# Performance work log

Hardware: AMD Instinct MI355X
Metric: run time of the kernel (lower is better)

## Reference

```python
import jax, jax.numpy as jnp
import numpy as np

N0, N1, N2 = 20000, 15000, 15000
N = N0 + N1 + N2            # total nodes
E = 800000                  # edges (avg degree 16)
H, C = 128, 64


def setup_inputs() -> dict:
    key = jax.random.key(0)
    ks = jax.random.split(key, 16)
    s = 0.05  # weight scale
    return {
        "feat0": jax.random.normal(ks[0], (N0, 512), jnp.float32),
        "feat1": jax.random.normal(ks[1], (N1, 256), jnp.float32),
        "feat2": jax.random.normal(ks[2], (N2, 128), jnp.float32),
        "W0": jax.random.normal(ks[3], (512, H), jnp.float32) * s,
        "b0": jnp.zeros((H,), jnp.float32),
        "W1": jax.random.normal(ks[4], (256, H), jnp.float32) * s,
        "b1": jnp.zeros((H,), jnp.float32),
        "W2": jax.random.normal(ks[5], (128, H), jnp.float32) * s,
        "b2": jnp.zeros((H,), jnp.float32),
        "bias_l0": jnp.zeros((H,), jnp.float32),
        "W_l1": jax.random.normal(ks[6], (H, H), jnp.float32) * s,
        "b_l1": jnp.zeros((H,), jnp.float32),
        "W_l2": jax.random.normal(ks[7], (H, C), jnp.float32) * s,
        "b_l2": jnp.zeros((C,), jnp.float32),
        "src": jax.random.randint(ks[8], (E,), 0, N, jnp.int32),
        "dst": jax.random.randint(ks[9], (E,), 0, N, jnp.int32),
    }


def _norms(src, dst):
    # DGL GraphConv norm='both': src side uses out-degree, dst side in-degree
    ones = jnp.ones((E,), jnp.float32)
    deg_out = jax.ops.segment_sum(ones, src, num_segments=N)
    deg_in = jax.ops.segment_sum(ones, dst, num_segments=N)
    return jnp.maximum(deg_out, 1.0) ** -0.5, jnp.maximum(deg_in, 1.0) ** -0.5


def _agg(h, src, dst, norm_src, norm_dst):
    # normalized sparse aggregation: D_in^{-1/2} A D_out^{-1/2} h
    m = (h * norm_src[:, None])[src]                     # [E, d] gather
    a = jax.ops.segment_sum(m, dst, num_segments=N)      # [N, d] scatter-add
    return a * norm_dst[:, None]


def reference(feat0, feat1, feat2, W0, b0, W1, b1, W2, b2,
              bias_l0, W_l1, b_l1, W_l2, b_l2, src, dst):
    # per-node-type linear projections, concatenated along node axis
    h = jnp.concatenate([feat0 @ W0 + b0,
                         feat1 @ W1 + b1,
                         feat2 @ W2 + b2], axis=0)       # [N, H]
    ns, nd = _norms(src, dst)
    # layer 0: GraphConv(weight=False) -> agg + bias + relu (dropout = eval identity)
    h = jax.nn.relu(_agg(h, src, dst, ns, nd) + bias_l0)
    # layer 1: agg + linear + relu
    h = jax.nn.relu(_agg(h, src, dst, ns, nd) @ W_l1 + b_l1)
    # layer 2: agg + linear (no activation)
    h = _agg(h, src, dst, ns, nd) @ W_l2 + b_l2          # [N, C]
    return h
```

## Files before the change

kernel.cpp:

```cpp
#include <hip/hip_runtime.h>
#include <hip/hip_fp16.h>

#define N_NODES 50000
#define N0_ 20000
#define N1_ 15000
#define N2_ 15000
#define E_EDGES 800000
#define H_ 128
#define C_ 64

#define PB0 ((N0_ + 63) / 64)
#define PB1 ((N1_ + 63) / 64)
#define PB2 ((N2_ + 63) / 64)
#define PB_TOTAL (PB0 + PB1 + PB2)
#define EB ((E_EDGES + 255) / 256)
#define SB ((N_NODES + 255) / 256)


template <int TN, bool BIAS, bool RELU, bool SCALE, typename OT>
__device__ __forceinline__ void gemm_block(
    const float* __restrict__ A, const float* __restrict__ W,
    const float* __restrict__ bias, const float* __restrict__ rowscale,
    OT* __restrict__ out, int M, int K, int m0, float* As, float* Bs) {
    constexpr int NJ = TN / 32;
    constexpr int TN4 = TN / 4;
    int tid = threadIdx.x;
    int tx = tid & 31;
    int ty = tid >> 5;

    float acc[8][NJ];
#pragma unroll
    for (int i = 0; i < 8; i++)
#pragma unroll
        for (int j = 0; j < NJ; j++) acc[i][j] = 0.f;

    for (int k0 = 0; k0 < K; k0 += 32) {
#pragma unroll
        for (int t0 = 0; t0 < 2; t0++) {
            int t = tid + t0 * 256;
            int row = t >> 3;
            int c = t & 7;
            float4 v = make_float4(0.f, 0.f, 0.f, 0.f);
            if (m0 + row < M) v = *reinterpret_cast<const float4*>(&A[(size_t)(m0 + row) * K + k0 + c * 4]);
            As[(c * 4 + 0) * 68 + row] = v.x;
            As[(c * 4 + 1) * 68 + row] = v.y;
            As[(c * 4 + 2) * 68 + row] = v.z;
            As[(c * 4 + 3) * 68 + row] = v.w;
        }
#pragma unroll
        for (int t0 = 0; t0 < 32 * TN4 / 256; t0++) {
            int t = tid + t0 * 256;
            int r = t / TN4;
            int c4 = t % TN4;
            *reinterpret_cast<float4*>(&Bs[r * TN + c4 * 4]) =
                *reinterpret_cast<const float4*>(&W[(size_t)(k0 + r) * TN + c4 * 4]);
        }
        __syncthreads();
#pragma unroll 8
        for (int k = 0; k < 32; k++) {
            float4 a0 = *reinterpret_cast<float4*>(&As[k * 68 + ty * 8]);
            float4 a1 = *reinterpret_cast<float4*>(&As[k * 68 + ty * 8 + 4]);
            float ar[8] = {a0.x, a0.y, a0.z, a0.w, a1.x, a1.y, a1.z, a1.w};
            float br[NJ];
#pragma unroll
            for (int j = 0; j < NJ; j++) br[j] = Bs[k * TN + tx + 32 * j];
#pragma unroll
            for (int i = 0; i < 8; i++)
#pragma unroll
                for (int j = 0; j < NJ; j++) acc[i][j] = fmaf(ar[i], br[j], acc[i][j]);
        }
        __syncthreads();
    }
#pragma unroll
    for (int i = 0; i < 8; i++) {
        int row = m0 + ty * 8 + i;
        if (row < M) {
            float sc = SCALE ? rowscale[row] : 1.f;
#pragma unroll
            for (int j = 0; j < NJ; j++) {
                float v = acc[i][j] + (BIAS ? bias[tx + 32 * j] : 0.f);
                if (RELU) v = fmaxf(v, 0.f);
                v *= sc;
                out[(size_t)row * TN + tx + 32 * j] = (OT)v;
            }
        }
    }
}


__global__ __launch_bounds__(256) void k1_proj_rank(
    const float* __restrict__ feat0, const float* __restrict__ feat1, const float* __restrict__ feat2,
    const float* __restrict__ W0, const float* __restrict__ b0,
    const float* __restrict__ W1, const float* __restrict__ b1,
    const float* __restrict__ W2, const float* __restrict__ b2,
    __half* __restrict__ h0h,
    const int* __restrict__ src, const int* __restrict__ dst,
    int* __restrict__ cnt, int* __restrict__ degO, int* __restrict__ rank) {
    __shared__ float As[32 * 68];
    __shared__ float Bs[32 * 128];
    int bid = blockIdx.x;
    if (bid < PB_TOTAL) {
        const float* A; const float* Wp; const float* bp; __half* op; int M, K, m0;
        if (bid < PB0) {
            A = feat0; Wp = W0; bp = b0; op = h0h; M = N0_; K = 512; m0 = bid * 64;
        } else if (bid < PB0 + PB1) {
            A = feat1; Wp = W1; bp = b1; op = h0h + (size_t)N0_ * H_; M = N1_; K = 256;
            m0 = (bid - PB0) * 64;
        } else {
            A = feat2; Wp = W2; bp = b2; op = h0h + (size_t)(N0_ + N1_) * H_; M = N2_; K = 128;
            m0 = (bid - PB0 - PB1) * 64;
        }
        gemm_block<128, true, false, false, __half>(A, Wp, bp, nullptr, op, M, K, m0, As, Bs);
    } else {
        int e = (bid - PB_TOTAL) * 256 + threadIdx.x;
        if (e < E_EDGES) {
            rank[e] = atomicAdd(&cnt[dst[e]], 1);
            atomicAdd(&degO[src[e]], 1);
        }
    }
}


__global__ __launch_bounds__(256) void scan1_kernel(
    const int* __restrict__ cnt, int* __restrict__ pre, int* __restrict__ blocksum) {
    __shared__ int buf[256];
    int t = threadIdx.x;
    int i = blockIdx.x * 256 + t;
    int tot = (i < N_NODES) ? cnt[i] : 0;
    buf[t] = tot;
    __syncthreads();
#pragma unroll
    for (int off = 1; off < 256; off <<= 1) {
        int v = (t >= off) ? buf[t - off] : 0;
        __syncthreads();
        buf[t] += v;
        __syncthreads();
    }
    if (i < N_NODES) pre[i] = buf[t] - tot;
    if (t == 255) blocksum[blockIdx.x] = buf[255];
}

__global__ __launch_bounds__(256) void scan2_kernel(
    const int* __restrict__ blocksum, int* __restrict__ blockoff, int* __restrict__ rowptr) {
    __shared__ int buf[256];
    int t = threadIdx.x;
    int v = (t < SB) ? blocksum[t] : 0;
    buf[t] = v;
    __syncthreads();
#pragma unroll
    for (int off = 1; off < 256; off <<= 1) {
        int u = (t >= off) ? buf[t - off] : 0;
        __syncthreads();
        buf[t] += u;
        __syncthreads();
    }
    if (t < SB) blockoff[t] = buf[t] - v;
    if (t == 255) rowptr[N_NODES] = buf[255];
}

__global__ __launch_bounds__(256) void scan3_kernel(
    const int* __restrict__ cnt, const int* __restrict__ degO, const int* __restrict__ pre,
    const int* __restrict__ blockoff, int* __restrict__ rowptr,
    float* __restrict__ ns, float* __restrict__ nd) {
    int i = blockIdx.x * 256 + threadIdx.x;
    if (i < N_NODES) {
        rowptr[i] = blockoff[blockIdx.x] + pre[i];
        ns[i] = rsqrtf(fmaxf((float)degO[i], 1.0f));
        nd[i] = rsqrtf(fmaxf((float)cnt[i], 1.0f));
    }
}


__global__ __launch_bounds__(256) void k2_fill(
    const int* __restrict__ src, const int* __restrict__ dst,
    const int* __restrict__ rowptr, const int* __restrict__ rank,
    int* __restrict__ col) {
    int e = blockIdx.x * 256 + threadIdx.x;
    if (e < E_EDGES) col[rowptr[dst[e]] + rank[e]] = src[e];
}


template <int NSLOAD, int EPI, int OUTH>
__global__ __launch_bounds__(256) void agg_h_kernel(
    const __half* __restrict__ h, const int* __restrict__ rowptr,
    const int* __restrict__ col, const float* __restrict__ ns,
    const float* __restrict__ nd, const float* __restrict__ bias,
    void* __restrict__ out) {
    int node = blockIdx.x * 4 + (threadIdx.x >> 6);
    if (node >= N_NODES) return;
    int lane = threadIdx.x & 63;
    int li = lane & 15;
    int g = lane >> 4;
    const uint4* __restrict__ h8 = (const uint4*)h;
    int beg = rowptr[node], end = rowptr[node + 1];
    float a0[8] = {0.f, 0.f, 0.f, 0.f, 0.f, 0.f, 0.f, 0.f};
    float a1[8] = {0.f, 0.f, 0.f, 0.f, 0.f, 0.f, 0.f, 0.f};
    union U8 { uint4 u; __half2 h2[4]; };
    int e = beg + g;
    for (; e + 4 < end; e += 8) {
        int s0 = col[e], s1 = col[e + 4];
        U8 u0, u1;
        u0.u = h8[(size_t)s0 * 16 + li];
        u1.u = h8[(size_t)s1 * 16 + li];
        float w0 = NSLOAD ? ns[s0] : 1.f;
        float w1 = NSLOAD ? ns[s1] : 1.f;
#pragma unroll
        for (int p = 0; p < 4; p++) {
            float2 f0 = __half22float2(u0.h2[p]);
            float2 f1 = __half22float2(u1.h2[p]);
            if (NSLOAD) {
                a0[2 * p] = fmaf(w0, f0.x, a0[2 * p]);
                a0[2 * p + 1] = fmaf(w0, f0.y, a0[2 * p + 1]);
                a1[2 * p] = fmaf(w1, f1.x, a1[2 * p]);
                a1[2 * p + 1] = fmaf(w1, f1.y, a1[2 * p + 1]);
            } else {
                a0[2 * p] += f0.x;
                a0[2 * p + 1] += f0.y;
                a1[2 * p] += f1.x;
                a1[2 * p + 1] += f1.y;
            }
        }
    }
    if (e < end) {
        int s = col[e];
        U8 u0;
        u0.u = h8[(size_t)s * 16 + li];
        float w0 = NSLOAD ? ns[s] : 1.f;
#pragma unroll
        for (int p = 0; p < 4; p++) {
            float2 f0 = __half22float2(u0.h2[p]);
            if (NSLOAD) {
                a0[2 * p] = fmaf(w0, f0.x, a0[2 * p]);
                a0[2 * p + 1] = fmaf(w0, f0.y, a0[2 * p + 1]);
            } else {
                a0[2 * p] += f0.x;
                a0[2 * p + 1] += f0.y;
            }
        }
    }
#pragma unroll
    for (int j = 0; j < 8; j++) {
        float v = a0[j] + a1[j];
        v += __shfl_xor(v, 32);
        v += __shfl_xor(v, 16);
        a0[j] = v;
    }
    if (lane < 16) {
        float w = nd[node];
#pragma unroll
        for (int j = 0; j < 8; j++) a0[j] *= w;
        if (EPI == 1) {
            float sc = ns[node];
#pragma unroll
            for (int j = 0; j < 8; j++)
                a0[j] = fmaxf(a0[j] + bias[li * 8 + j], 0.f) * sc;
        }
        if (OUTH) {
            union { uint4 u; __half hh[8]; } cv;
#pragma unroll
            for (int j = 0; j < 8; j++) cv.hh[j] = __float2half(a0[j]);
            ((uint4*)out)[(size_t)node * 16 + li] = cv.u;
        } else {
            float4* o4 = (float4*)out;
            o4[(size_t)node * 32 + li * 2] = make_float4(a0[0], a0[1], a0[2], a0[3]);
            o4[(size_t)node * 32 + li * 2 + 1] = make_float4(a0[4], a0[5], a0[6], a0[7]);
        }
    }
}


template <int CH, int NSLOAD, int EPI>
__global__ __launch_bounds__(256) void agg_kernel(
    const float* __restrict__ h, const int* __restrict__ rowptr,
    const int* __restrict__ col, const float* __restrict__ ns,
    const float* __restrict__ nd, const float* __restrict__ bias,
    float* __restrict__ out) {
    constexpr int L = CH / 4;
    constexpr int EPW = 64 / L;
    int node = blockIdx.x * 4 + (threadIdx.x >> 6);
    if (node >= N_NODES) return;
    int lane = threadIdx.x & 63;
    int li = lane & (L - 1);
    int g = lane / L;
    const float4* __restrict__ h4 = (const float4*)h;
    int beg = rowptr[node], end = rowptr[node + 1];
    float4 a0 = make_float4(0.f, 0.f, 0.f, 0.f);
    float4 a1 = a0;
    int e = beg + g;
    for (; e + EPW < end; e += 2 * EPW) {
        int s0 = col[e], s1 = col[e + EPW];
        float4 v0 = h4[(size_t)s0 * L + li];
        float4 v1 = h4[(size_t)s1 * L + li];
        if (NSLOAD) {
            float w0 = ns[s0], w1 = ns[s1];
            a0.x = fmaf(w0, v0.x, a0.x); a0.y = fmaf(w0, v0.y, a0.y);
            a0.z = fmaf(w0, v0.z, a0.z); a0.w = fmaf(w0, v0.w, a0.w);
            a1.x = fmaf(w1, v1.x, a1.x); a1.y = fmaf(w1, v1.y, a1.y);
            a1.z = fmaf(w1, v1.z, a1.z); a1.w = fmaf(w1, v1.w, a1.w);
        } else {
            a0.x += v0.x; a0.y += v0.y; a0.z += v0.z; a0.w += v0.w;
            a1.x += v1.x; a1.y += v1.y; a1.z += v1.z; a1.w += v1.w;
        }
    }
    if (e < end) {
        int s = col[e];
        float4 v = h4[(size_t)s * L + li];
        if (NSLOAD) {
            float w = ns[s];
            a0.x = fmaf(w, v.x, a0.x); a0.y = fmaf(w, v.y, a0.y);
            a0.z = fmaf(w, v.z, a0.z); a0.w = fmaf(w, v.w, a0.w);
        } else {
            a0.x += v.x; a0.y += v.y; a0.z += v.z; a0.w += v.w;
        }
    }
    float4 acc = make_float4(a0.x + a1.x, a0.y + a1.y, a0.z + a1.z, a0.w + a1.w);
#pragma unroll
    for (int off = 32; off >= L; off >>= 1) {
        acc.x += __shfl_xor(acc.x, off);
        acc.y += __shfl_xor(acc.y, off);
        acc.z += __shfl_xor(acc.z, off);
        acc.w += __shfl_xor(acc.w, off);
    }
    if (lane < L) {
        float w = nd[node];
        acc.x *= w; acc.y *= w; acc.z *= w; acc.w *= w;
        if (EPI == 2) {
            float4 b = ((const float4*)bias)[lane];
            acc.x += b.x; acc.y += b.y; acc.z += b.z; acc.w += b.w;
        }
        ((float4*)out)[(size_t)node * L + lane] = acc;
    }
}


template <int TN, bool BIAS, bool RELU, bool SCALE>
__global__ __launch_bounds__(256) void gemm_kernel(
    const float* __restrict__ A, const float* __restrict__ W,
    const float* __restrict__ bias, const float* __restrict__ rowscale,
    float* __restrict__ out, int M, int K) {
    __shared__ float As[32 * 68];
    __shared__ float Bs[32 * TN];
    gemm_block<TN, BIAS, RELU, SCALE, float>(A, W, bias, rowscale, out, M, K, blockIdx.x * 64, As, Bs);
}


extern "C" void kernel_launch(void* const* d_in, const int* in_sizes, int n_in,
                              void* d_out, int out_size, void* d_ws, size_t ws_size,
                              hipStream_t stream) {
    const float* feat0 = (const float*)d_in[0];
    const float* feat1 = (const float*)d_in[1];
    const float* feat2 = (const float*)d_in[2];
    const float* W0 = (const float*)d_in[3];
    const float* b0 = (const float*)d_in[4];
    const float* W1 = (const float*)d_in[5];
    const float* b1 = (const float*)d_in[6];
    const float* W2 = (const float*)d_in[7];
    const float* b2 = (const float*)d_in[8];
    const float* bias_l0 = (const float*)d_in[9];
    const float* W_l1 = (const float*)d_in[10];
    const float* b_l1 = (const float*)d_in[11];
    const float* W_l2 = (const float*)d_in[12];
    const float* b_l2 = (const float*)d_in[13];
    const int* src = (const int*)d_in[14];
    const int* dst = (const int*)d_in[15];
    float* out = (float*)d_out;

    char* ws = (char*)d_ws;
    size_t off = 0;
    auto alloc = [&](size_t bytes) {
        size_t cur = off;
        off += (bytes + 255) & ~(size_t)255;
        return cur;
    };
    size_t hA_off = alloc((size_t)N_NODES * H_ * 4);
    size_t hB_off = alloc((size_t)N_NODES * H_ * 4);
    size_t h0h_off = alloc((size_t)N_NODES * H_ * 2);
    size_t h1h_off = alloc((size_t)N_NODES * H_ * 2);
    size_t cnt_off = alloc((size_t)N_NODES * 4);
    size_t degO_off = alloc((size_t)N_NODES * 4);
    size_t ns_off = alloc((size_t)N_NODES * 4);
    size_t nd_off = alloc((size_t)N_NODES * 4);
    size_t rowptr_off = alloc((size_t)(N_NODES + 1) * 4);
    size_t rank_off = alloc((size_t)E_EDGES * 4);
    size_t col_off = alloc((size_t)E_EDGES * 4);
    size_t pre_off = alloc((size_t)N_NODES * 4);
    size_t bsum_off = alloc((size_t)SB * 4);
    size_t boff_off = alloc((size_t)SB * 4);

    float* hA = (float*)(ws + hA_off);
    float* hB = (float*)(ws + hB_off);
    __half* h0h = (__half*)(ws + h0h_off);
    __half* h1h = (__half*)(ws + h1h_off);
    int* cnt = (int*)(ws + cnt_off);
    int* degO = (int*)(ws + degO_off);
    float* ns = (float*)(ws + ns_off);
    float* nd = (float*)(ws + nd_off);
    int* rowptr = (int*)(ws + rowptr_off);
    int* rank = (int*)(ws + rank_off);
    int* col = (int*)(ws + col_off);
    int* pre = (int*)(ws + pre_off);
    int* bsum = (int*)(ws + bsum_off);
    int* boff = (int*)(ws + boff_off);

    hipMemsetAsync(ws + cnt_off, 0, ns_off - cnt_off, stream);

    k1_proj_rank<<<PB_TOTAL + EB, 256, 0, stream>>>(
        feat0, feat1, feat2, W0, b0, W1, b1, W2, b2, h0h, src, dst, cnt, degO, rank);
    scan1_kernel<<<SB, 256, 0, stream>>>(cnt, pre, bsum);
    scan2_kernel<<<1, 256, 0, stream>>>(bsum, boff, rowptr);
    scan3_kernel<<<SB, 256, 0, stream>>>(cnt, degO, pre, boff, rowptr, ns, nd);
    k2_fill<<<EB, 256, 0, stream>>>(src, dst, rowptr, rank, col);

    const int AGB = (N_NODES + 3) / 4;
    agg_h_kernel<1, 1, 1><<<AGB, 256, 0, stream>>>(h0h, rowptr, col, ns, nd, bias_l0, h1h);
    agg_h_kernel<0, 0, 0><<<AGB, 256, 0, stream>>>(h1h, rowptr, col, ns, nd, nullptr, hA);
    gemm_kernel<128, true, true, true><<<(N_NODES + 63) / 64, 256, 0, stream>>>(
        hA, W_l1, b_l1, ns, hB, N_NODES, 128);
    gemm_kernel<64, false, false, false><<<(N_NODES + 63) / 64, 256, 0, stream>>>(
        hB, W_l2, nullptr, nullptr, hA, N_NODES, 128);
    agg_kernel<64, 0, 2><<<AGB, 256, 0, stream>>>(hA, rowptr, col, ns, nd, b_l2, out);
}
```

Measured before the change: 269.3 us.

## Enlarge GEMM row tiles to 128 and store layer-2 features in half precision

```diff
diff --git a/kernel.cpp b/kernel.cpp
--- a/kernel.cpp
+++ b/kernel.cpp
@@ -9,9 +9,9 @@
 #define H_ 128
 #define C_ 64
 
-#define PB0 ((N0_ + 63) / 64)
-#define PB1 ((N1_ + 63) / 64)
-#define PB2 ((N2_ + 63) / 64)
+#define PB0 ((N0_ + 127) / 128)
+#define PB1 ((N1_ + 127) / 128)
+#define PB2 ((N2_ + 127) / 128)
 #define PB_TOTAL (PB0 + PB1 + PB2)
 #define EB ((E_EDGES + 255) / 256)
 #define SB ((N_NODES + 255) / 256)
@@ -22,11 +22,11 @@
     const float* __restrict__ A, const float* __restrict__ W,
     const float* __restrict__ bias, const float* __restrict__ rowscale,
     OT* __restrict__ out, int M, int K, int m0, float* As, float* Bs) {
-    constexpr int NJ = TN / 32;
+    constexpr int NJ = TN / 16;
     constexpr int TN4 = TN / 4;
     int tid = threadIdx.x;
-    int tx = tid & 31;
-    int ty = tid >> 5;
+    int tx = tid & 15;
+    int ty = tid >> 4;
 
     float acc[8][NJ];
 #pragma unroll
@@ -36,16 +36,16 @@
 
     for (int k0 = 0; k0 < K; k0 += 32) {
 #pragma unroll
-        for (int t0 = 0; t0 < 2; t0++) {
+        for (int t0 = 0; t0 < 4; t0++) {
             int t = tid + t0 * 256;
             int row = t >> 3;
             int c = t & 7;
             float4 v = make_float4(0.f, 0.f, 0.f, 0.f);
             if (m0 + row < M) v = *reinterpret_cast<const float4*>(&A[(size_t)(m0 + row) * K + k0 + c * 4]);
-            As[(c * 4 + 0) * 68 + row] = v.x;
-            As[(c * 4 + 1) * 68 + row] = v.y;
-            As[(c * 4 + 2) * 68 + row] = v.z;
-            As[(c * 4 + 3) * 68 + row] = v.w;
+            As[(c * 4 + 0) * 132 + row] = v.x;
+            As[(c * 4 + 1) * 132 + row] = v.y;
+            As[(c * 4 + 2) * 132 + row] = v.z;
+            As[(c * 4 + 3) * 132 + row] = v.w;
         }
 #pragma unroll
         for (int t0 = 0; t0 < 32 * TN4 / 256; t0++) {
@@ -58,12 +58,12 @@
         __syncthreads();
 #pragma unroll 8
         for (int k = 0; k < 32; k++) {
-            float4 a0 = *reinterpret_cast<float4*>(&As[k * 68 + ty * 8]);
-            float4 a1 = *reinterpret_cast<float4*>(&As[k * 68 + ty * 8 + 4]);
+            float4 a0 = *reinterpret_cast<float4*>(&As[k * 132 + ty * 8]);
+            float4 a1 = *reinterpret_cast<float4*>(&As[k * 132 + ty * 8 + 4]);
             float ar[8] = {a0.x, a0.y, a0.z, a0.w, a1.x, a1.y, a1.z, a1.w};
             float br[NJ];
 #pragma unroll
-            for (int j = 0; j < NJ; j++) br[j] = Bs[k * TN + tx + 32 * j];
+            for (int j = 0; j < NJ; j++) br[j] = Bs[k * TN + tx + 16 * j];
 #pragma unroll
             for (int i = 0; i < 8; i++)
 #pragma unroll
@@ -78,10 +78,10 @@
             float sc = SCALE ? rowscale[row] : 1.f;
 #pragma unroll
             for (int j = 0; j < NJ; j++) {
-                float v = acc[i][j] + (BIAS ? bias[tx + 32 * j] : 0.f);
+                float v = acc[i][j] + (BIAS ? bias[tx + 16 * j] : 0.f);
                 if (RELU) v = fmaxf(v, 0.f);
                 v *= sc;
-                out[(size_t)row * TN + tx + 32 * j] = (OT)v;
+                out[(size_t)row * TN + tx + 16 * j] = (OT)v;
             }
         }
     }
@@ -96,19 +96,19 @@
     __half* __restrict__ h0h,
     const int* __restrict__ src, const int* __restrict__ dst,
     int* __restrict__ cnt, int* __restrict__ degO, int* __restrict__ rank) {
-    __shared__ float As[32 * 68];
+    __shared__ float As[32 * 132];
     __shared__ float Bs[32 * 128];
     int bid = blockIdx.x;
     if (bid < PB_TOTAL) {
         const float* A; const float* Wp; const float* bp; __half* op; int M, K, m0;
         if (bid < PB0) {
-            A = feat0; Wp = W0; bp = b0; op = h0h; M = N0_; K = 512; m0 = bid * 64;
+            A = feat0; Wp = W0; bp = b0; op = h0h; M = N0_; K = 512; m0 = bid * 128;
         } else if (bid < PB0 + PB1) {
             A = feat1; Wp = W1; bp = b1; op = h0h + (size_t)N0_ * H_; M = N1_; K = 256;
-            m0 = (bid - PB0) * 64;
+            m0 = (bid - PB0) * 128;
         } else {
             A = feat2; Wp = W2; bp = b2; op = h0h + (size_t)(N0_ + N1_) * H_; M = N2_; K = 128;
-            m0 = (bid - PB0 - PB1) * 64;
+            m0 = (bid - PB0 - PB1) * 128;
         }
         gemm_block<128, true, false, false, __half>(A, Wp, bp, nullptr, op, M, K, m0, As, Bs);
     } else {
@@ -180,28 +180,30 @@
 }
 
 
-template <int NSLOAD, int EPI, int OUTH>
+template <int CH, int NSLOAD, int EPI, int OUTH>
 __global__ __launch_bounds__(256) void agg_h_kernel(
     const __half* __restrict__ h, const int* __restrict__ rowptr,
     const int* __restrict__ col, const float* __restrict__ ns,
     const float* __restrict__ nd, const float* __restrict__ bias,
     void* __restrict__ out) {
+    constexpr int L = CH / 8;
+    constexpr int EPW = 64 / L;
     int node = blockIdx.x * 4 + (threadIdx.x >> 6);
     if (node >= N_NODES) return;
     int lane = threadIdx.x & 63;
-    int li = lane & 15;
-    int g = lane >> 4;
+    int li = lane & (L - 1);
+    int g = lane / L;
     const uint4* __restrict__ h8 = (const uint4*)h;
     int beg = rowptr[node], end = rowptr[node + 1];
     float a0[8] = {0.f, 0.f, 0.f, 0.f, 0.f, 0.f, 0.f, 0.f};
     float a1[8] = {0.f, 0.f, 0.f, 0.f, 0.f, 0.f, 0.f, 0.f};
     union U8 { uint4 u; __half2 h2[4]; };
     int e = beg + g;
-    for (; e + 4 < end; e += 8) {
-        int s0 = col[e], s1 = col[e + 4];
+    for (; e + EPW < end; e += 2 * EPW) {
+        int s0 = col[e], s1 = col[e + EPW];
         U8 u0, u1;
-        u0.u = h8[(size_t)s0 * 16 + li];
-        u1.u = h8[(size_t)s1 * 16 + li];
+        u0.u = h8[(size_t)s0 * L + li];
+        u1.u = h8[(size_t)s1 * L + li];
         float w0 = NSLOAD ? ns[s0] : 1.f;
         float w1 = NSLOAD ? ns[s1] : 1.f;
 #pragma unroll
@@ -224,7 +226,7 @@
     if (e < end) {
         int s = col[e];
         U8 u0;
-        u0.u = h8[(size_t)s * 16 + li];
+        u0.u = h8[(size_t)s * L + li];
         float w0 = NSLOAD ? ns[s] : 1.f;
 #pragma unroll
         for (int p = 0; p < 4; p++) {
@@ -241,11 +243,11 @@
 #pragma unroll
     for (int j = 0; j < 8; j++) {
         float v = a0[j] + a1[j];
-        v += __shfl_xor(v, 32);
-        v += __shfl_xor(v, 16);
+#pragma unroll
+        for (int off = 32; off >= L; off >>= 1) v += __shfl_xor(v, off);
         a0[j] = v;
     }
-    if (lane < 16) {
+    if (lane < L) {
         float w = nd[node];
 #pragma unroll
         for (int j = 0; j < 8; j++) a0[j] *= w;
@@ -254,93 +256,32 @@
 #pragma unroll
             for (int j = 0; j < 8; j++)
                 a0[j] = fmaxf(a0[j] + bias[li * 8 + j], 0.f) * sc;
+        } else if (EPI == 2) {
+#pragma unroll
+            for (int j = 0; j < 8; j++) a0[j] += bias[li * 8 + j];
         }
         if (OUTH) {
             union { uint4 u; __half hh[8]; } cv;
 #pragma unroll
             for (int j = 0; j < 8; j++) cv.hh[j] = __float2half(a0[j]);
-            ((uint4*)out)[(size_t)node * 16 + li] = cv.u;
+            ((uint4*)out)[(size_t)node * L + li] = cv.u;
         } else {
             float4* o4 = (float4*)out;
-            o4[(size_t)node * 32 + li * 2] = make_float4(a0[0], a0[1], a0[2], a0[3]);
-            o4[(size_t)node * 32 + li * 2 + 1] = make_float4(a0[4], a0[5], a0[6], a0[7]);
-        }
-    }
-}
-
-
-template <int CH, int NSLOAD, int EPI>
-__global__ __launch_bounds__(256) void agg_kernel(
-    const float* __restrict__ h, const int* __restrict__ rowptr,
-    const int* __restrict__ col, const float* __restrict__ ns,
-    const float* __restrict__ nd, const float* __restrict__ bias,
-    float* __restrict__ out) {
-    constexpr int L = CH / 4;
-    constexpr int EPW = 64 / L;
-    int node = blockIdx.x * 4 + (threadIdx.x >> 6);
-    if (node >= N_NODES) return;
-    int lane = threadIdx.x & 63;
-    int li = lane & (L - 1);
-    int g = lane / L;
-    const float4* __restrict__ h4 = (const float4*)h;
-    int beg = rowptr[node], end = rowptr[node + 1];
-    float4 a0 = make_float4(0.f, 0.f, 0.f, 0.f);
-    float4 a1 = a0;
-    int e = beg + g;
-    for (; e + EPW < end; e += 2 * EPW) {
-        int s0 = col[e], s1 = col[e + EPW];
-        float4 v0 = h4[(size_t)s0 * L + li];
-        float4 v1 = h4[(size_t)s1 * L + li];
-        if (NSLOAD) {
-            float w0 = ns[s0], w1 = ns[s1];
-            a0.x = fmaf(w0, v0.x, a0.x); a0.y = fmaf(w0, v0.y, a0.y);
-            a0.z = fmaf(w0, v0.z, a0.z); a0.w = fmaf(w0, v0.w, a0.w);
-            a1.x = fmaf(w1, v1.x, a1.x); a1.y = fmaf(w1, v1.y, a1.y);
-            a1.z = fmaf(w1, v1.z, a1.z); a1.w = fmaf(w1, v1.w, a1.w);
-        } else {
-            a0.x += v0.x; a0.y += v0.y; a0.z += v0.z; a0.w += v0.w;
-            a1.x += v1.x; a1.y += v1.y; a1.z += v1.z; a1.w += v1.w;
-        }
-    }
-    if (e < end) {
-        int s = col[e];
-        float4 v = h4[(size_t)s * L + li];
-        if (NSLOAD) {
-            float w = ns[s];
-            a0.x = fmaf(w, v.x, a0.x); a0.y = fmaf(w, v.y, a0.y);
-            a0.z = fmaf(w, v.z, a0.z); a0.w = fmaf(w, v.w, a0.w);
-        } else {
-            a0.x += v.x; a0.y += v.y; a0.z += v.z; a0.w += v.w;
-        }
-    }
-    float4 acc = make_float4(a0.x + a1.x, a0.y + a1.y, a0.z + a1.z, a0.w + a1.w);
-#pragma unroll
-    for (int off = 32; off >= L; off >>= 1) {
-        acc.x += __shfl_xor(acc.x, off);
-        acc.y += __shfl_xor(acc.y, off);
-        acc.z += __shfl_xor(acc.z, off);
-        acc.w += __shfl_xor(acc.w, off);
-    }
-    if (lane < L) {
-        float w = nd[node];
-        acc.x *= w; acc.y *= w; acc.z *= w; acc.w *= w;
-        if (EPI == 2) {
-            float4 b = ((const float4*)bias)[lane];
-            acc.x += b.x; acc.y += b.y; acc.z += b.z; acc.w += b.w;
-        }
-        ((float4*)out)[(size_t)node * L + lane] = acc;
-    }
-}
-
-
-template <int TN, bool BIAS, bool RELU, bool SCALE>
+            o4[(size_t)node * (CH / 4) + li * 2] = make_float4(a0[0], a0[1], a0[2], a0[3]);
+            o4[(size_t)node * (CH / 4) + li * 2 + 1] = make_float4(a0[4], a0[5], a0[6], a0[7]);
+        }
+    }
+}
+
+
+template <int TN, bool BIAS, bool RELU, bool SCALE, typename OT>
 __global__ __launch_bounds__(256) void gemm_kernel(
     const float* __restrict__ A, const float* __restrict__ W,
     const float* __restrict__ bias, const float* __restrict__ rowscale,
-    float* __restrict__ out, int M, int K) {
-    __shared__ float As[32 * 68];
+    OT* __restrict__ out, int M, int K) {
+    __shared__ float As[32 * 132];
     __shared__ float Bs[32 * TN];
-    gemm_block<TN, BIAS, RELU, SCALE, float>(A, W, bias, rowscale, out, M, K, blockIdx.x * 64, As, Bs);
+    gemm_block<TN, BIAS, RELU, SCALE, OT>(A, W, bias, rowscale, out, M, K, blockIdx.x * 128, As, Bs);
 }
 
 
@@ -376,6 +317,7 @@
     size_t hB_off = alloc((size_t)N_NODES * H_ * 4);
     size_t h0h_off = alloc((size_t)N_NODES * H_ * 2);
     size_t h1h_off = alloc((size_t)N_NODES * H_ * 2);
+    size_t h2h_off = alloc((size_t)N_NODES * C_ * 2);
     size_t cnt_off = alloc((size_t)N_NODES * 4);
     size_t degO_off = alloc((size_t)N_NODES * 4);
     size_t ns_off = alloc((size_t)N_NODES * 4);
@@ -391,6 +333,7 @@
     float* hB = (float*)(ws + hB_off);
     __half* h0h = (__half*)(ws + h0h_off);
     __half* h1h = (__half*)(ws + h1h_off);
+    __half* h2h = (__half*)(ws + h2h_off);
     int* cnt = (int*)(ws + cnt_off);
     int* degO = (int*)(ws + degO_off);
     float* ns = (float*)(ws + ns_off);
@@ -412,11 +355,11 @@
     k2_fill<<<EB, 256, 0, stream>>>(src, dst, rowptr, rank, col);
 
     const int AGB = (N_NODES + 3) / 4;
-    agg_h_kernel<1, 1, 1><<<AGB, 256, 0, stream>>>(h0h, rowptr, col, ns, nd, bias_l0, h1h);
-    agg_h_kernel<0, 0, 0><<<AGB, 256, 0, stream>>>(h1h, rowptr, col, ns, nd, nullptr, hA);
-    gemm_kernel<128, true, true, true><<<(N_NODES + 63) / 64, 256, 0, stream>>>(
+    agg_h_kernel<128, 1, 1, 1><<<AGB, 256, 0, stream>>>(h0h, rowptr, col, ns, nd, bias_l0, h1h);
+    agg_h_kernel<128, 0, 0, 0><<<AGB, 256, 0, stream>>>(h1h, rowptr, col, ns, nd, nullptr, hA);
+    gemm_kernel<128, true, true, true, float><<<(N_NODES + 127) / 128, 256, 0, stream>>>(
         hA, W_l1, b_l1, ns, hB, N_NODES, 128);
-    gemm_kernel<64, false, false, false><<<(N_NODES + 63) / 64, 256, 0, stream>>>(
-        hB, W_l2, nullptr, nullptr, hA, N_NODES, 128);
-    agg_kernel<64, 0, 2><<<AGB, 256, 0, stream>>>(hA, rowptr, col, ns, nd, b_l2, out);
-}
+    gemm_kernel<64, false, false, false, __half><<<(N_NODES + 127) / 128, 256, 0, stream>>>(
+        hB, W_l2, nullptr, nullptr, h2h, N_NODES, 128);
+    agg_h_kernel<64, 0, 2, 0><<<AGB, 256, 0, stream>>>(h2h, rowptr, col, ns, nd, b_l2, out);
+}
```

Result: slower. 308.6 us (+14.6%).
